# Kernel optimization log

Measured on AMD Instinct MI355X. Metric: run time of the kernel, lower is better.

The kernel has to match this reference:

```python
import jax, jax.numpy as jnp
import numpy as np

DIM, N_HEADS, N_KV, HEAD_DIM = 5120, 40, 8, 128
MAX_BS, MAX_SEQ = 8, 4096
BSZ, SEQLEN, START_POS = 8, 1, 4095


def setup_inputs() -> dict:
    key = jax.random.key(0)
    ks = jax.random.split(key, 12)
    x = jax.random.normal(ks[0], (BSZ, SEQLEN, DIM), jnp.float32)
    # RoPE angles for positions [START_POS, START_POS+SEQLEN)
    inv_freq = 1.0 / (10000.0 ** (np.arange(0, HEAD_DIM, 2, dtype=np.float32) / HEAD_DIM))
    t = np.arange(START_POS, START_POS + SEQLEN, dtype=np.float32)
    ang = np.outer(t, inv_freq)  # [seqlen, head_dim//2]
    freqs_cis = jnp.asarray(np.stack([np.cos(ang), np.sin(ang)], axis=-1), jnp.float32)
    cache_k = jax.random.normal(ks[1], (MAX_BS, MAX_SEQ, N_KV, HEAD_DIM), jnp.float32)
    cache_v = jax.random.normal(ks[2], (MAX_BS, MAX_SEQ, N_KV, HEAD_DIM), jnp.float32)
    s = 0.02
    wq = jax.random.normal(ks[3], (DIM, N_HEADS * HEAD_DIM), jnp.float32) * s
    bq = jax.random.normal(ks[4], (N_HEADS * HEAD_DIM,), jnp.float32) * s
    wk = jax.random.normal(ks[5], (DIM, N_KV * HEAD_DIM), jnp.float32) * s
    bk = jax.random.normal(ks[6], (N_KV * HEAD_DIM,), jnp.float32) * s
    wv = jax.random.normal(ks[7], (DIM, N_KV * HEAD_DIM), jnp.float32) * s
    bv = jax.random.normal(ks[8], (N_KV * HEAD_DIM,), jnp.float32) * s
    wo = jax.random.normal(ks[9], (N_HEADS * HEAD_DIM, DIM), jnp.float32) * s
    bo = jax.random.normal(ks[10], (DIM,), jnp.float32) * s
    return dict(x=x, start_pos=START_POS, freqs_cis=freqs_cis, cache_k=cache_k,
                cache_v=cache_v, wq=wq, bq=bq, wk=wk, bk=bk, wv=wv, bv=bv, wo=wo, bo=bo)


def _apply_rope(xq, xk, freqs_cis):
    # x*: [b, s, h, hd]; freqs_cis: [s, hd//2, 2] (cos, sin)
    cos = freqs_cis[None, :, None, :, 0]
    sin = freqs_cis[None, :, None, :, 1]
    def rot(x):
        xr = x.reshape(*x.shape[:-1], HEAD_DIM // 2, 2)
        xe, xo = xr[..., 0], xr[..., 1]
        out = jnp.stack([xe * cos - xo * sin, xe * sin + xo * cos], axis=-1)
        return out.reshape(x.shape)
    return rot(xq), rot(xk)


def reference(x, start_pos, freqs_cis, cache_k, cache_v, wq, bq, wk, bk, wv, bv, wo, bo):
    bsz, seqlen, _ = x.shape
    n_rep = N_HEADS // N_KV
    xq = (x @ wq + bq).reshape(bsz, seqlen, N_HEADS, HEAD_DIM)
    xk = (x @ wk + bk).reshape(bsz, seqlen, N_KV, HEAD_DIM)
    xv = (x @ wv + bv).reshape(bsz, seqlen, N_KV, HEAD_DIM)
    xq, xk = _apply_rope(xq, xk, freqs_cis)
    # KV-cache scatter (in-place write in the original)
    cache_k = jax.lax.dynamic_update_slice(cache_k, xk, (0, start_pos, 0, 0))
    cache_v = jax.lax.dynamic_update_slice(cache_v, xv, (0, start_pos, 0, 0))
    klen = start_pos + seqlen
    keys = cache_k[:bsz, :klen]    # [b, t, n_kv, hd]
    values = cache_v[:bsz, :klen]
    # GQA attention without materializing the repeat_kv expansion (same math)
    qg = xq.reshape(bsz, seqlen, N_KV, n_rep, HEAD_DIM)
    scale = 1.0 / np.sqrt(HEAD_DIM)
    scores = jnp.einsum('bsgrd,btgd->bgrst', qg, keys) * scale  # [b,g,r,s,t]
    probs = jax.nn.softmax(scores.astype(jnp.float32), axis=-1).astype(x.dtype)
    out = jnp.einsum('bgrst,btgd->bsgrd', probs, values)
    out = out.reshape(bsz, seqlen, N_HEADS * HEAD_DIM)
    return out @ wo + bo
```

## Files before the change

kernel.cpp:

```cpp
#include <hip/hip_runtime.h>
#include <hip/hip_bf16.h>
#include <math.h>

#define DIM   5120
#define NH    40
#define NKV   8
#define HD    128
#define BS    8
#define KLEN  4096
#define NEWT  4095
#define NREP  5

#define ODQKV 7168
#define NKC   32
#define KCH   (DIM / NKC)

#define NCHB  64
#define CH_T  (KLEN / NCHB)
#define NPART NCHB

#define WS_Q       0
#define WS_K       (WS_Q + BS * DIM)
#define WS_V       (WS_K + BS * NKV * HD)
#define WS_ATTN    (WS_V + BS * NKV * HD)
#define WS_SCRATCH (WS_ATTN + BS * DIM)

__device__ __forceinline__ void gload_lds16(const float* g, float* l) {
  __builtin_amdgcn_global_load_lds(
      (const __attribute__((address_space(1))) void*)(unsigned long long)g,
      (__attribute__((address_space(3))) void*)(unsigned int)(unsigned long long)l,
      16, 0, 0);
}

__global__ __launch_bounds__(256) void qkv_partial_k(
    const float* __restrict__ x, const float* __restrict__ wq,
    const float* __restrict__ wk, const float* __restrict__ wv,
    float* __restrict__ part) {
  const int cb = blockIdx.x % 14;
  const int kc = blockIdx.x / 14;
  const int c0 = cb * 512 + threadIdx.x * 2;

  const float* w; int OD, j;
  if (c0 < 5120)      { w = wq; OD = 5120; j = c0; }
  else if (c0 < 6144) { w = wk; OD = 1024; j = c0 - 5120; }
  else                { w = wv; OD = 1024; j = c0 - 6144; }

  const int i0 = kc * KCH;
  float ax[BS], ay[BS];
#pragma unroll
  for (int b = 0; b < BS; ++b) { ax[b] = 0.f; ay[b] = 0.f; }

  const float* wp = w + (size_t)i0 * OD + j;
  const float* xp = x + i0;
#pragma unroll 4
  for (int ii = 0; ii < KCH; ++ii) {
    const float2 wv2 = *(const float2*)&wp[(size_t)ii * OD];
#pragma unroll
    for (int b = 0; b < BS; ++b) {
      const float xb = xp[b * DIM + ii];
      ax[b] = fmaf(xb, wv2.x, ax[b]);
      ay[b] = fmaf(xb, wv2.y, ay[b]);
    }
  }
#pragma unroll
  for (int b = 0; b < BS; ++b)
    *(float2*)&part[((size_t)kc * BS + b) * ODQKV + c0] = make_float2(ax[b], ay[b]);
}

__global__ __launch_bounds__(256) void qkv_reduce_k(
    const float* __restrict__ part, const float* __restrict__ bq,
    const float* __restrict__ bk, const float* __restrict__ bv,
    const float* __restrict__ fc, float* __restrict__ qws,
    float* __restrict__ kws, float* __restrict__ vws) {
  int g = blockIdx.x * 256 + threadIdx.x;
  if (g >= BS * (ODQKV / 2)) return;
  int b  = g / (ODQKV / 2);
  int cp = g - b * (ODQKV / 2);
  int c0 = cp * 2;

  float sx = 0.f, sy = 0.f;
  for (int kc = 0; kc < NKC; ++kc) {
    const float2 p = *(const float2*)&part[((size_t)kc * BS + b) * ODQKV + c0];
    sx += p.x; sy += p.y;
  }

  const float scale = 0.088388347648318447f;
  if (c0 < 5120) {
    sx += bq[c0]; sy += bq[c0 + 1];
    int jf = (c0 & 127) >> 1;
    float cs = fc[2 * jf], sn = fc[2 * jf + 1];
    qws[b * DIM + c0]     = (sx * cs - sy * sn) * scale;
    qws[b * DIM + c0 + 1] = (sx * sn + sy * cs) * scale;
  } else if (c0 < 6144) {
    int jj = c0 - 5120;
    sx += bk[jj]; sy += bk[jj + 1];
    int jf = (jj & 127) >> 1;
    float cs = fc[2 * jf], sn = fc[2 * jf + 1];
    kws[b * NKV * HD + jj]     = sx * cs - sy * sn;
    kws[b * NKV * HD + jj + 1] = sx * sn + sy * cs;
  } else {
    int jj = c0 - 6144;
    vws[b * NKV * HD + jj]     = sx + bv[jj];
    vws[b * NKV * HD + jj + 1] = sy + bv[jj + 1];
  }
}

__global__ __launch_bounds__(256) void attn_partial_k(
    const float* __restrict__ ck, const float* __restrict__ cv,
    const float* __restrict__ qws, const float* __restrict__ kws,
    const float* __restrict__ vws, float* __restrict__ pM,
    float* __restrict__ pL, float* __restrict__ pO) {
  const int blk   = blockIdx.x;
  const int chunk = blk & (NCHB - 1);
  const int bh    = blk / NCHB;
  const int h     = bh & (NKV - 1);
  const int b     = bh / NKV;
  const int tid   = threadIdx.x;
  const int w     = tid >> 6;
  const int lane  = tid & 63;
  const int g     = lane >> 4;
  const int sl    = lane & 15;
  const int t0    = chunk * CH_T;

  __shared__ float K_lds[CH_T * HD];
  __shared__ float s_lds[CH_T * NREP];
  __shared__ float red[NREP * 8];
  __shared__ float Msh[NREP], Lsh[NREP];

  {
    const int hv  = lane >> 5;
    const int l32 = lane & 31;
#pragma unroll
    for (int ii = 0; ii < 8; ++ii) {
      const int i  = w * 8 + ii;
      const int r  = 2 * i + hv;
      const int tg = t0 + r;
      const float* rowb = (tg == NEWT)
          ? (kws + (b * NKV + h) * HD)
          : (ck + (((size_t)b * KLEN + tg) * NKV + h) * HD);
      const float* src = rowb + 4 * ((l32 - (r & 3)) & 31);
      gload_lds16(src, &K_lds[i * 256]);
    }
  }

  float4 qa[NREP], qb[NREP];
#pragma unroll
  for (int rr = 0; rr < NREP; ++rr) {
    const float* qp = &qws[b * DIM + (h * NREP + rr) * HD + 8 * sl];
    qa[rr] = *(const float4*)qp;
    qb[rr] = *(const float4*)(qp + 4);
  }

  __syncthreads();

#pragma unroll
  for (int j = 0; j < 4; ++j) {
    const int r  = w * 16 + j * 4 + g;
    const int x0 = (sl * 8 + 4 * g) & 127;
    const float4 k0 = *(const float4*)&K_lds[r * HD + x0];
    const float4 k1 = *(const float4*)&K_lds[r * HD + ((x0 + 4) & 127)];
    float s[NREP];
#pragma unroll
    for (int rr = 0; rr < NREP; ++rr) {
      s[rr] = qa[rr].x * k0.x + qa[rr].y * k0.y + qa[rr].z * k0.z + qa[rr].w * k0.w
            + qb[rr].x * k1.x + qb[rr].y * k1.y + qb[rr].z * k1.z + qb[rr].w * k1.w;
    }
#pragma unroll
    for (int off = 1; off < 16; off <<= 1) {
#pragma unroll
      for (int rr = 0; rr < NREP; ++rr) s[rr] += __shfl_xor(s[rr], off, 64);
    }
    float sv = (sl == 0) ? s[0] : (sl == 1) ? s[1] : (sl == 2) ? s[2]
             : (sl == 3) ? s[3] : s[4];
    if (sl < NREP) s_lds[r * NREP + sl] = sv;
  }
  __syncthreads();

  if (tid < NREP * 8) {
    const int rr = tid >> 3, seg = tid & 7;
    float mx = -1e30f;
#pragma unroll
    for (int k = 0; k < 8; ++k) mx = fmaxf(mx, s_lds[(seg * 8 + k) * NREP + rr]);
    red[tid] = mx;
  }
  __syncthreads();
  if (tid < NREP) {
    float mx = red[tid * 8];
#pragma unroll
    for (int k = 1; k < 8; ++k) mx = fmaxf(mx, red[tid * 8 + k]);
    Msh[tid] = mx;
  }
  __syncthreads();
  for (int idx = tid; idx < CH_T * NREP; idx += 256)
    s_lds[idx] = __expf(s_lds[idx] - Msh[idx % NREP]);
  __syncthreads();
  if (tid < NREP * 8) {
    const int rr = tid >> 3, seg = tid & 7;
    float sm = 0.f;
#pragma unroll
    for (int k = 0; k < 8; ++k) sm += s_lds[(seg * 8 + k) * NREP + rr];
    red[tid] = sm;
  }
  __syncthreads();
  if (tid < NREP) {
    float L = 0.f;
#pragma unroll
    for (int k = 0; k < 8; ++k) L += red[tid * 8 + k];
    Lsh[tid] = L;
  }

  float o[NREP][8];
#pragma unroll
  for (int rr = 0; rr < NREP; ++rr)
#pragma unroll
    for (int j = 0; j < 8; ++j) o[rr][j] = 0.f;

  const bool tailw = (chunk == NCHB - 1) && (w == 3);
  const int  jmax  = tailw ? 3 : 4;
  {
    const float* vp = cv + (((size_t)b * KLEN + (t0 + w * 16 + g)) * NKV + h) * HD + 8 * sl;
#pragma unroll
    for (int j = 0; j < jmax; ++j) {
      const float4 va = *(const float4*)vp;
      const float4 vb = *(const float4*)(vp + 4);
      const int r = w * 16 + j * 4 + g;
      float p[NREP];
#pragma unroll
      for (int rr = 0; rr < NREP; ++rr) p[rr] = s_lds[r * NREP + rr];
      const float vv[8] = {va.x, va.y, va.z, va.w, vb.x, vb.y, vb.z, vb.w};
#pragma unroll
      for (int rr = 0; rr < NREP; ++rr)
#pragma unroll
        for (int jj = 0; jj < 8; ++jj) o[rr][jj] = fmaf(p[rr], vv[jj], o[rr][jj]);
      vp += (size_t)4 * NKV * HD;
    }
    if (tailw) {
      const int r  = 60 + g;
      const int tg = t0 + r;
      const float* vr = (tg == NEWT) ? (vws + (b * NKV + h) * HD)
                                     : (cv + (((size_t)b * KLEN + tg) * NKV + h) * HD);
      const float4 va = *(const float4*)(vr + 8 * sl);
      const float4 vb = *(const float4*)(vr + 8 * sl + 4);
      float p[NREP];
#pragma unroll
      for (int rr = 0; rr < NREP; ++rr) p[rr] = s_lds[r * NREP + rr];
      const float vv[8] = {va.x, va.y, va.z, va.w, vb.x, vb.y, vb.z, vb.w};
#pragma unroll
      for (int rr = 0; rr < NREP; ++rr)
#pragma unroll
        for (int jj = 0; jj < 8; ++jj) o[rr][jj] = fmaf(p[rr], vv[jj], o[rr][jj]);
    }
  }

#pragma unroll
  for (int off = 16; off <= 32; off <<= 1) {
#pragma unroll
    for (int rr = 0; rr < NREP; ++rr)
#pragma unroll
      for (int jj = 0; jj < 8; ++jj) o[rr][jj] += __shfl_xor(o[rr][jj], off, 64);
  }

  float* smO = K_lds;
  if (g == 0) {
#pragma unroll
    for (int rr = 0; rr < NREP; ++rr) {
      float* sp = &smO[(w * NREP + rr) * HD + 8 * sl];
      *(float4*)sp       = make_float4(o[rr][0], o[rr][1], o[rr][2], o[rr][3]);
      *(float4*)(sp + 4) = make_float4(o[rr][4], o[rr][5], o[rr][6], o[rr][7]);
    }
  }
  __syncthreads();

  if (tid < HD) {
    const int d  = tid;
    const int pb = bh * NCHB + chunk;
#pragma unroll
    for (int rr = 0; rr < NREP; ++rr) {
      float acc = smO[rr * HD + d] + smO[(NREP + rr) * HD + d]
                + smO[(2 * NREP + rr) * HD + d] + smO[(3 * NREP + rr) * HD + d];
      pO[((size_t)pb * NREP + rr) * HD + d] = acc;
      if (d == 0) { pM[pb * NREP + rr] = Msh[rr]; pL[pb * NREP + rr] = Lsh[rr]; }
    }
  }
}

__global__ __launch_bounds__(256) void attn_combine_k(
    const float* __restrict__ pM, const float* __restrict__ pL,
    const float* __restrict__ pO, float* __restrict__ attn) {
  const int bh  = blockIdx.x;
  const int h   = bh & (NKV - 1);
  const int b   = bh / NKV;
  const int tid = threadIdx.x;
  __shared__ float ml[NREP * NPART], ll[NREP * NPART];
  __shared__ float wgt[NREP * NPART];
  __shared__ float Linv[NREP];

  for (int idx = tid; idx < NREP * NPART; idx += 256) {
    int r = idx / NPART, w = idx - r * NPART;
    ml[idx] = pM[(bh * NPART + w) * NREP + r];
    ll[idx] = pL[(bh * NPART + w) * NREP + r];
  }
  __syncthreads();
  for (int idx = tid; idx < NREP * NPART; idx += 256) {
    int r = idx / NPART;
    float M = -1e30f;
    for (int w = 0; w < NPART; ++w) M = fmaxf(M, ml[r * NPART + w]);
    float e = __expf(ml[idx] - M);
    wgt[idx] = e;
    ll[idx] *= e;
  }
  __syncthreads();
  if (tid < NREP) {
    float L = 0.f;
    for (int w = 0; w < NPART; ++w) L += ll[tid * NPART + w];
    Linv[tid] = 1.f / L;
  }
  __syncthreads();

  for (int oidx = tid; oidx < NREP * HD; oidx += 256) {
    int r = oidx >> 7, d = oidx & 127;
    float acc = 0.f;
    for (int w = 0; w < NPART; ++w)
      acc += wgt[r * NPART + w] * pO[((size_t)(bh * NPART + w) * NREP + r) * HD + d];
    attn[b * DIM + (h * NREP + r) * HD + d] = acc * Linv[r];
  }
}

__global__ __launch_bounds__(256) void out_partial_k(
    const float* __restrict__ attn, const float* __restrict__ wo,
    float* __restrict__ part) {
  const int cb = blockIdx.x % 10;
  const int kc = blockIdx.x / 10;
  const int c0 = cb * 512 + threadIdx.x * 2;

  const int i0 = kc * KCH;
  float ax[BS], ay[BS];
#pragma unroll
  for (int b = 0; b < BS; ++b) { ax[b] = 0.f; ay[b] = 0.f; }

  const float* wp = wo + (size_t)i0 * DIM + c0;
  const float* xp = attn + i0;
#pragma unroll 4
  for (int ii = 0; ii < KCH; ++ii) {
    const float2 wv2 = *(const float2*)&wp[(size_t)ii * DIM];
#pragma unroll
    for (int b = 0; b < BS; ++b) {
      const float xb = xp[b * DIM + ii];
      ax[b] = fmaf(xb, wv2.x, ax[b]);
      ay[b] = fmaf(xb, wv2.y, ay[b]);
    }
  }
#pragma unroll
  for (int b = 0; b < BS; ++b)
    *(float2*)&part[((size_t)kc * BS + b) * DIM + c0] = make_float2(ax[b], ay[b]);
}

__global__ __launch_bounds__(256) void out_reduce_k(
    const float* __restrict__ part, const float* __restrict__ bo,
    float* __restrict__ out) {
  int g = blockIdx.x * 256 + threadIdx.x;
  if (g >= BS * DIM) return;
  int b = g / DIM, c = g - b * DIM;
  float s = 0.f;
  for (int kc = 0; kc < NKC; ++kc) s += part[((size_t)kc * BS + b) * DIM + c];
  out[g] = s + bo[c];
}

extern "C" void kernel_launch(void* const* d_in, const int* in_sizes, int n_in,
                              void* d_out, int out_size, void* d_ws, size_t ws_size,
                              hipStream_t stream) {
  const float* x  = (const float*)d_in[0];
  const float* fc = (const float*)d_in[2];
  const float* ck = (const float*)d_in[3];
  const float* cv = (const float*)d_in[4];
  const float* wq = (const float*)d_in[5];
  const float* bq = (const float*)d_in[6];
  const float* wk = (const float*)d_in[7];
  const float* bk = (const float*)d_in[8];
  const float* wv = (const float*)d_in[9];
  const float* bv = (const float*)d_in[10];
  const float* wo = (const float*)d_in[11];
  const float* bo = (const float*)d_in[12];

  float* ws      = (float*)d_ws;
  float* qws     = ws + WS_Q;
  float* kws     = ws + WS_K;
  float* vws     = ws + WS_V;
  float* attn    = ws + WS_ATTN;
  float* scratch = ws + WS_SCRATCH;

  qkv_partial_k<<<14 * NKC, 256, 0, stream>>>(x, wq, wk, wv, scratch);
  qkv_reduce_k<<<(BS * (ODQKV / 2) + 255) / 256, 256, 0, stream>>>(
      scratch, bq, bk, bv, fc, qws, kws, vws);

  float* pM = scratch;
  float* pL = pM + 64 * NPART * NREP;
  float* pO = pL + 64 * NPART * NREP;
  attn_partial_k<<<64 * NCHB, 256, 0, stream>>>(ck, cv, qws, kws, vws, pM, pL, pO);
  attn_combine_k<<<64, 256, 0, stream>>>(pM, pL, pO, attn);

  out_partial_k<<<10 * NKC, 256, 0, stream>>>(attn, wo, scratch);
  out_reduce_k<<<(BS * DIM + 255) / 256, 256, 0, stream>>>(scratch, bo, (float*)d_out);
}
```

Before: 154.1 us.

## Replace async LDS K load with padded register copy and per-row score dot products

Drops the global_load_lds async copy with its swizzle and instead stages K through registers into a padded LDS tile (stride 132) to avoid bank conflicts. The QK scores are restructured so each lane owns one key row and each wave covers a 32-dim slice, with partial sums written to an extra LDS buffer and reduced across the four waves. This removes the 16-lane shuffle reduction and the Q register preload, at the cost of more LDS, an extra reduction pass, Q read from global/cache inside the loop, and an added barrier before reusing K_lds.

```diff
diff --git a/kernel.cpp b/kernel.cpp
--- a/kernel.cpp
+++ b/kernel.cpp
@@ -15,22 +15,16 @@
 #define NKC   32
 #define KCH   (DIM / NKC)
 
-#define NCHB  64
-#define CH_T  (KLEN / NCHB)
-#define NPART NCHB
+#define NCHUNK 64
+#define CH_T   (KLEN / NCHUNK)
+#define NPART  NCHUNK
+#define KPAD   132
 
 #define WS_Q       0
 #define WS_K       (WS_Q + BS * DIM)
 #define WS_V       (WS_K + BS * NKV * HD)
 #define WS_ATTN    (WS_V + BS * NKV * HD)
 #define WS_SCRATCH (WS_ATTN + BS * DIM)
-
-__device__ __forceinline__ void gload_lds16(const float* g, float* l) {
-  __builtin_amdgcn_global_load_lds(
-      (const __attribute__((address_space(1))) void*)(unsigned long long)g,
-      (__attribute__((address_space(3))) void*)(unsigned int)(unsigned long long)l,
-      16, 0, 0);
-}
 
 __global__ __launch_bounds__(256) void qkv_partial_k(
     const float* __restrict__ x, const float* __restrict__ wq,
@@ -111,69 +105,65 @@
     const float* __restrict__ vws, float* __restrict__ pM,
     float* __restrict__ pL, float* __restrict__ pO) {
   const int blk   = blockIdx.x;
-  const int chunk = blk & (NCHB - 1);
-  const int bh    = blk / NCHB;
+  const int chunk = blk & (NCHUNK - 1);
+  const int bh    = blk / NCHUNK;
   const int h     = bh & (NKV - 1);
   const int b     = bh / NKV;
   const int tid   = threadIdx.x;
   const int w     = tid >> 6;
   const int lane  = tid & 63;
-  const int g     = lane >> 4;
-  const int sl    = lane & 15;
   const int t0    = chunk * CH_T;
 
-  __shared__ float K_lds[CH_T * HD];
+  __shared__ float K_lds[CH_T * KPAD];
+  __shared__ float spart[4 * CH_T * NREP];
   __shared__ float s_lds[CH_T * NREP];
   __shared__ float red[NREP * 8];
   __shared__ float Msh[NREP], Lsh[NREP];
 
   {
-    const int hv  = lane >> 5;
-    const int l32 = lane & 31;
-#pragma unroll
-    for (int ii = 0; ii < 8; ++ii) {
-      const int i  = w * 8 + ii;
-      const int r  = 2 * i + hv;
-      const int tg = t0 + r;
-      const float* rowb = (tg == NEWT)
-          ? (kws + (b * NKV + h) * HD)
-          : (ck + (((size_t)b * KLEN + tg) * NKV + h) * HD);
-      const float* src = rowb + 4 * ((l32 - (r & 3)) & 31);
-      gload_lds16(src, &K_lds[i * 256]);
-    }
-  }
-
-  float4 qa[NREP], qb[NREP];
-#pragma unroll
-  for (int rr = 0; rr < NREP; ++rr) {
-    const float* qp = &qws[b * DIM + (h * NREP + rr) * HD + 8 * sl];
-    qa[rr] = *(const float4*)qp;
-    qb[rr] = *(const float4*)(qp + 4);
-  }
-
-  __syncthreads();
-
-#pragma unroll
-  for (int j = 0; j < 4; ++j) {
-    const int r  = w * 16 + j * 4 + g;
-    const int x0 = (sl * 8 + 4 * g) & 127;
-    const float4 k0 = *(const float4*)&K_lds[r * HD + x0];
-    const float4 k1 = *(const float4*)&K_lds[r * HD + ((x0 + 4) & 127)];
+    const int rb = tid >> 5;
+    const int d0 = (tid & 31) * 4;
+#pragma unroll
+    for (int p = 0; p < 8; ++p) {
+      const int row = p * 8 + rb;
+      const int tg  = t0 + row;
+      const float* src = (tg == NEWT)
+          ? &kws[(b * NKV + h) * HD]
+          : &ck[(((size_t)b * KLEN + tg) * NKV + h) * HD];
+      *(float4*)&K_lds[row * KPAD + d0] = *(const float4*)&src[d0];
+    }
+  }
+  __syncthreads();
+
+  {
+    const int row = lane;
     float s[NREP];
 #pragma unroll
-    for (int rr = 0; rr < NREP; ++rr) {
-      s[rr] = qa[rr].x * k0.x + qa[rr].y * k0.y + qa[rr].z * k0.z + qa[rr].w * k0.w
-            + qb[rr].x * k1.x + qb[rr].y * k1.y + qb[rr].z * k1.z + qb[rr].w * k1.w;
-    }
-#pragma unroll
-    for (int off = 1; off < 16; off <<= 1) {
-#pragma unroll
-      for (int rr = 0; rr < NREP; ++rr) s[rr] += __shfl_xor(s[rr], off, 64);
-    }
-    float sv = (sl == 0) ? s[0] : (sl == 1) ? s[1] : (sl == 2) ? s[2]
-             : (sl == 3) ? s[3] : s[4];
-    if (sl < NREP) s_lds[r * NREP + sl] = sv;
-  }
+    for (int r = 0; r < NREP; ++r) s[r] = 0.f;
+    const float* qb = &qws[b * DIM + h * NREP * HD];
+    const int dbase = w * 32;
+#pragma unroll
+    for (int c = 0; c < 8; ++c) {
+      const int d0 = dbase + c * 4;
+      const float4 k4 = *(const float4*)&K_lds[row * KPAD + d0];
+#pragma unroll
+      for (int r = 0; r < NREP; ++r) {
+        const float4 q4 = *(const float4*)&qb[r * HD + d0];
+        s[r] = fmaf(k4.x, q4.x,
+               fmaf(k4.y, q4.y,
+               fmaf(k4.z, q4.z,
+               fmaf(k4.w, q4.w, s[r]))));
+      }
+    }
+#pragma unroll
+    for (int r = 0; r < NREP; ++r)
+      spart[(w * CH_T + row) * NREP + r] = s[r];
+  }
+  __syncthreads();
+
+  for (int idx = tid; idx < CH_T * NREP; idx += 256)
+    s_lds[idx] = spart[idx] + spart[CH_T * NREP + idx]
+               + spart[2 * CH_T * NREP + idx] + spart[3 * CH_T * NREP + idx];
   __syncthreads();
 
   if (tid < NREP * 8) {
@@ -209,13 +199,15 @@
     Lsh[tid] = L;
   }
 
+  const int g  = lane >> 4;
+  const int sl = lane & 15;
   float o[NREP][8];
 #pragma unroll
   for (int rr = 0; rr < NREP; ++rr)
 #pragma unroll
     for (int j = 0; j < 8; ++j) o[rr][j] = 0.f;
 
-  const bool tailw = (chunk == NCHB - 1) && (w == 3);
+  const bool tailw = (chunk == NCHUNK - 1) && (w == 3);
   const int  jmax  = tailw ? 3 : 4;
   {
     const float* vp = cv + (((size_t)b * KLEN + (t0 + w * 16 + g)) * NKV + h) * HD + 8 * sl;
@@ -260,6 +252,7 @@
       for (int jj = 0; jj < 8; ++jj) o[rr][jj] += __shfl_xor(o[rr][jj], off, 64);
   }
 
+  __syncthreads();
   float* smO = K_lds;
   if (g == 0) {
 #pragma unroll
@@ -273,7 +266,7 @@
 
   if (tid < HD) {
     const int d  = tid;
-    const int pb = bh * NCHB + chunk;
+    const int pb = bh * NCHUNK + chunk;
 #pragma unroll
     for (int rr = 0; rr < NREP; ++rr) {
       float acc = smO[rr * HD + d] + smO[(NREP + rr) * HD + d]
@@ -396,7 +389,7 @@
   float* pM = scratch;
   float* pL = pM + 64 * NPART * NREP;
   float* pO = pL + 64 * NPART * NREP;
-  attn_partial_k<<<64 * NCHB, 256, 0, stream>>>(ck, cv, qws, kws, vws, pM, pL, pO);
+  attn_partial_k<<<64 * NCHUNK, 256, 0, stream>>>(ck, cv, qws, kws, vws, pM, pL, pO);
   attn_combine_k<<<64, 256, 0, stream>>>(pM, pL, pO, attn);
 
   out_partial_k<<<10 * NKC, 256, 0, stream>>>(attn, wo, scratch);
```

Measured after the change: 163.9 us. +6.4%, slower.

## Load K directly to registers, prefetch V early, split combine per head

Applied to the files above, without the earlier changes.

The attention partial kernel no longer stages the K chunk into LDS with global_load_lds. Each thread reads its K rows straight into registers, and the V rows are issued as register loads before the QK computation so their latency overlaps the score and softmax phases. An empty asm statement keeps the V values live. The combine kernel is split into one block per (batch, kv head, rep) with 128 threads, which removes the serial loops and extra shared-memory passes. The cost is higher register pressure in the partial kernel and more small blocks in the combine step.

```diff
diff --git a/kernel.cpp b/kernel.cpp
--- a/kernel.cpp
+++ b/kernel.cpp
@@ -15,22 +15,15 @@
 #define NKC   32
 #define KCH   (DIM / NKC)
 
-#define NCHB  64
-#define CH_T  (KLEN / NCHB)
-#define NPART NCHB
+#define NCHUNK 64
+#define CH_T   (KLEN / NCHUNK)
+#define NPART  NCHUNK
 
 #define WS_Q       0
 #define WS_K       (WS_Q + BS * DIM)
 #define WS_V       (WS_K + BS * NKV * HD)
 #define WS_ATTN    (WS_V + BS * NKV * HD)
 #define WS_SCRATCH (WS_ATTN + BS * DIM)
-
-__device__ __forceinline__ void gload_lds16(const float* g, float* l) {
-  __builtin_amdgcn_global_load_lds(
-      (const __attribute__((address_space(1))) void*)(unsigned long long)g,
-      (__attribute__((address_space(3))) void*)(unsigned int)(unsigned long long)l,
-      16, 0, 0);
-}
 
 __global__ __launch_bounds__(256) void qkv_partial_k(
     const float* __restrict__ x, const float* __restrict__ wq,
@@ -111,8 +104,8 @@
     const float* __restrict__ vws, float* __restrict__ pM,
     float* __restrict__ pL, float* __restrict__ pO) {
   const int blk   = blockIdx.x;
-  const int chunk = blk & (NCHB - 1);
-  const int bh    = blk / NCHB;
+  const int chunk = blk & (NCHUNK - 1);
+  const int bh    = blk / NCHUNK;
   const int h     = bh & (NKV - 1);
   const int b     = bh / NKV;
   const int tid   = threadIdx.x;
@@ -121,26 +114,29 @@
   const int g     = lane >> 4;
   const int sl    = lane & 15;
   const int t0    = chunk * CH_T;
-
-  __shared__ float K_lds[CH_T * HD];
+  const int rw0   = w * 16;
+
   __shared__ float s_lds[CH_T * NREP];
   __shared__ float red[NREP * 8];
   __shared__ float Msh[NREP], Lsh[NREP];
-
+  __shared__ float smO[4 * NREP * HD];
+
+  const int r3  = rw0 + 12 + g;
+  const int tg3 = t0 + r3;
+
+  float4 vA[4], vB[4];
   {
-    const int hv  = lane >> 5;
-    const int l32 = lane & 31;
-#pragma unroll
-    for (int ii = 0; ii < 8; ++ii) {
-      const int i  = w * 8 + ii;
-      const int r  = 2 * i + hv;
-      const int tg = t0 + r;
-      const float* rowb = (tg == NEWT)
-          ? (kws + (b * NKV + h) * HD)
-          : (ck + (((size_t)b * KLEN + tg) * NKV + h) * HD);
-      const float* src = rowb + 4 * ((l32 - (r & 3)) & 31);
-      gload_lds16(src, &K_lds[i * 256]);
-    }
+    const float* vp = cv + (((size_t)b * KLEN + (t0 + rw0 + g)) * NKV + h) * HD + 8 * sl;
+#pragma unroll
+    for (int j = 0; j < 3; ++j) {
+      vA[j] = *(const float4*)vp;
+      vB[j] = *(const float4*)(vp + 4);
+      vp += (size_t)4 * NKV * HD;
+    }
+    const float* vr3 = (tg3 == NEWT) ? (vws + (b * NKV + h) * HD)
+                                     : (cv + (((size_t)b * KLEN + tg3) * NKV + h) * HD);
+    vA[3] = *(const float4*)(vr3 + 8 * sl);
+    vB[3] = *(const float4*)(vr3 + 8 * sl + 4);
   }
 
   float4 qa[NREP], qb[NREP];
@@ -151,29 +147,35 @@
     qb[rr] = *(const float4*)(qp + 4);
   }
 
-  __syncthreads();
-
-#pragma unroll
-  for (int j = 0; j < 4; ++j) {
-    const int r  = w * 16 + j * 4 + g;
-    const int x0 = (sl * 8 + 4 * g) & 127;
-    const float4 k0 = *(const float4*)&K_lds[r * HD + x0];
-    const float4 k1 = *(const float4*)&K_lds[r * HD + ((x0 + 4) & 127)];
-    float s[NREP];
-#pragma unroll
-    for (int rr = 0; rr < NREP; ++rr) {
-      s[rr] = qa[rr].x * k0.x + qa[rr].y * k0.y + qa[rr].z * k0.z + qa[rr].w * k0.w
-            + qb[rr].x * k1.x + qb[rr].y * k1.y + qb[rr].z * k1.z + qb[rr].w * k1.w;
-    }
-#pragma unroll
-    for (int off = 1; off < 16; off <<= 1) {
-#pragma unroll
-      for (int rr = 0; rr < NREP; ++rr) s[rr] += __shfl_xor(s[rr], off, 64);
-    }
-    float sv = (sl == 0) ? s[0] : (sl == 1) ? s[1] : (sl == 2) ? s[2]
-             : (sl == 3) ? s[3] : s[4];
-    if (sl < NREP) s_lds[r * NREP + sl] = sv;
-  }
+  {
+    const float* kp = ck + (((size_t)b * KLEN + (t0 + rw0 + g)) * NKV + h) * HD + 8 * sl;
+#pragma unroll
+    for (int i = 0; i < 4; ++i) {
+      const float* kr = kp;
+      if (i == 3 && tg3 == NEWT) kr = kws + (b * NKV + h) * HD + 8 * sl;
+      const float4 ka = *(const float4*)kr;
+      const float4 kb = *(const float4*)(kr + 4);
+      kp += (size_t)4 * NKV * HD;
+      float s[NREP];
+#pragma unroll
+      for (int rr = 0; rr < NREP; ++rr) {
+        s[rr] = qa[rr].x * ka.x + qa[rr].y * ka.y + qa[rr].z * ka.z + qa[rr].w * ka.w
+              + qb[rr].x * kb.x + qb[rr].y * kb.y + qb[rr].z * kb.z + qb[rr].w * kb.w;
+      }
+#pragma unroll
+      for (int off = 1; off < 16; off <<= 1) {
+#pragma unroll
+        for (int rr = 0; rr < NREP; ++rr) s[rr] += __shfl_xor(s[rr], off, 64);
+      }
+      const int tl = rw0 + 4 * i + g;
+      float sv = (sl == 0) ? s[0] : (sl == 1) ? s[1] : (sl == 2) ? s[2]
+               : (sl == 3) ? s[3] : s[4];
+      if (sl < NREP) s_lds[tl * NREP + sl] = sv;
+    }
+  }
+#pragma unroll
+  for (int j = 0; j < 4; ++j)
+    asm volatile("" :: "v"(vA[j].x), "v"(vA[j].w), "v"(vB[j].x), "v"(vB[j].w));
   __syncthreads();
 
   if (tid < NREP * 8) {
@@ -213,43 +215,20 @@
 #pragma unroll
   for (int rr = 0; rr < NREP; ++rr)
 #pragma unroll
-    for (int j = 0; j < 8; ++j) o[rr][j] = 0.f;
-
-  const bool tailw = (chunk == NCHB - 1) && (w == 3);
-  const int  jmax  = tailw ? 3 : 4;
-  {
-    const float* vp = cv + (((size_t)b * KLEN + (t0 + w * 16 + g)) * NKV + h) * HD + 8 * sl;
-#pragma unroll
-    for (int j = 0; j < jmax; ++j) {
-      const float4 va = *(const float4*)vp;
-      const float4 vb = *(const float4*)(vp + 4);
-      const int r = w * 16 + j * 4 + g;
-      float p[NREP];
-#pragma unroll
-      for (int rr = 0; rr < NREP; ++rr) p[rr] = s_lds[r * NREP + rr];
-      const float vv[8] = {va.x, va.y, va.z, va.w, vb.x, vb.y, vb.z, vb.w};
-#pragma unroll
-      for (int rr = 0; rr < NREP; ++rr)
-#pragma unroll
-        for (int jj = 0; jj < 8; ++jj) o[rr][jj] = fmaf(p[rr], vv[jj], o[rr][jj]);
-      vp += (size_t)4 * NKV * HD;
-    }
-    if (tailw) {
-      const int r  = 60 + g;
-      const int tg = t0 + r;
-      const float* vr = (tg == NEWT) ? (vws + (b * NKV + h) * HD)
-                                     : (cv + (((size_t)b * KLEN + tg) * NKV + h) * HD);
-      const float4 va = *(const float4*)(vr + 8 * sl);
-      const float4 vb = *(const float4*)(vr + 8 * sl + 4);
-      float p[NREP];
-#pragma unroll
-      for (int rr = 0; rr < NREP; ++rr) p[rr] = s_lds[r * NREP + rr];
-      const float vv[8] = {va.x, va.y, va.z, va.w, vb.x, vb.y, vb.z, vb.w};
-#pragma unroll
-      for (int rr = 0; rr < NREP; ++rr)
-#pragma unroll
-        for (int jj = 0; jj < 8; ++jj) o[rr][jj] = fmaf(p[rr], vv[jj], o[rr][jj]);
-    }
+    for (int jj = 0; jj < 8; ++jj) o[rr][jj] = 0.f;
+
+#pragma unroll
+  for (int j = 0; j < 4; ++j) {
+    const int r = rw0 + j * 4 + g;
+    float p[NREP];
+#pragma unroll
+    for (int rr = 0; rr < NREP; ++rr) p[rr] = s_lds[r * NREP + rr];
+    const float vv[8] = {vA[j].x, vA[j].y, vA[j].z, vA[j].w,
+                         vB[j].x, vB[j].y, vB[j].z, vB[j].w};
+#pragma unroll
+    for (int rr = 0; rr < NREP; ++rr)
+#pragma unroll
+      for (int jj = 0; jj < 8; ++jj) o[rr][jj] = fmaf(p[rr], vv[jj], o[rr][jj]);
   }
 
 #pragma unroll
@@ -260,7 +239,6 @@
       for (int jj = 0; jj < 8; ++jj) o[rr][jj] += __shfl_xor(o[rr][jj], off, 64);
   }
 
-  float* smO = K_lds;
   if (g == 0) {
 #pragma unroll
     for (int rr = 0; rr < NREP; ++rr) {
@@ -273,7 +251,7 @@
 
   if (tid < HD) {
     const int d  = tid;
-    const int pb = bh * NCHB + chunk;
+    const int pb = bh * NPART + chunk;
 #pragma unroll
     for (int rr = 0; rr < NREP; ++rr) {
       float acc = smO[rr * HD + d] + smO[(NREP + rr) * HD + d]
@@ -284,46 +262,32 @@
   }
 }
 
-__global__ __launch_bounds__(256) void attn_combine_k(
+__global__ __launch_bounds__(128) void attn_combine_k(
     const float* __restrict__ pM, const float* __restrict__ pL,
     const float* __restrict__ pO, float* __restrict__ attn) {
-  const int bh  = blockIdx.x;
+  const int bhr = blockIdx.x;
+  const int r   = bhr % NREP;
+  const int bh  = bhr / NREP;
   const int h   = bh & (NKV - 1);
   const int b   = bh / NKV;
-  const int tid = threadIdx.x;
-  __shared__ float ml[NREP * NPART], ll[NREP * NPART];
-  __shared__ float wgt[NREP * NPART];
-  __shared__ float Linv[NREP];
-
-  for (int idx = tid; idx < NREP * NPART; idx += 256) {
-    int r = idx / NPART, w = idx - r * NPART;
-    ml[idx] = pM[(bh * NPART + w) * NREP + r];
-    ll[idx] = pL[(bh * NPART + w) * NREP + r];
-  }
-  __syncthreads();
-  for (int idx = tid; idx < NREP * NPART; idx += 256) {
-    int r = idx / NPART;
-    float M = -1e30f;
-    for (int w = 0; w < NPART; ++w) M = fmaxf(M, ml[r * NPART + w]);
-    float e = __expf(ml[idx] - M);
-    wgt[idx] = e;
-    ll[idx] *= e;
-  }
-  __syncthreads();
-  if (tid < NREP) {
-    float L = 0.f;
-    for (int w = 0; w < NPART; ++w) L += ll[tid * NPART + w];
-    Linv[tid] = 1.f / L;
-  }
-  __syncthreads();
-
-  for (int oidx = tid; oidx < NREP * HD; oidx += 256) {
-    int r = oidx >> 7, d = oidx & 127;
-    float acc = 0.f;
-    for (int w = 0; w < NPART; ++w)
-      acc += wgt[r * NPART + w] * pO[((size_t)(bh * NPART + w) * NREP + r) * HD + d];
-    attn[b * DIM + (h * NREP + r) * HD + d] = acc * Linv[r];
-  }
+  const int d   = threadIdx.x;
+
+  __shared__ float ml[NPART], ll[NPART];
+  if (d < NPART) {
+    ml[d] = pM[(bh * NPART + d) * NREP + r];
+    ll[d] = pL[(bh * NPART + d) * NREP + r];
+  }
+  __syncthreads();
+
+  float M = -1e30f;
+  for (int w2 = 0; w2 < NPART; ++w2) M = fmaxf(M, ml[w2]);
+  float L = 0.f, acc = 0.f;
+  for (int w2 = 0; w2 < NPART; ++w2) {
+    const float e = __expf(ml[w2] - M);
+    L  = fmaf(e, ll[w2], L);
+    acc = fmaf(e, pO[((size_t)(bh * NPART + w2) * NREP + r) * HD + d], acc);
+  }
+  attn[b * DIM + (h * NREP + r) * HD + d] = acc / L;
 }
 
 __global__ __launch_bounds__(256) void out_partial_k(
@@ -396,8 +360,8 @@
   float* pM = scratch;
   float* pL = pM + 64 * NPART * NREP;
   float* pO = pL + 64 * NPART * NREP;
-  attn_partial_k<<<64 * NCHB, 256, 0, stream>>>(ck, cv, qws, kws, vws, pM, pL, pO);
-  attn_combine_k<<<64, 256, 0, stream>>>(pM, pL, pO, attn);
+  attn_partial_k<<<64 * NCHUNK, 256, 0, stream>>>(ck, cv, qws, kws, vws, pM, pL, pO);
+  attn_combine_k<<<64 * NREP, 128, 0, stream>>>(pM, pL, pO, attn);
 
   out_partial_k<<<10 * NKC, 256, 0, stream>>>(attn, wo, scratch);
   out_reduce_k<<<(BS * DIM + 255) / 256, 256, 0, stream>>>(scratch, bo, (float*)d_out);
```

Result: faster. 143.0 us (-7.2%).
